# Kernel optimization log

Hardware: AMD Instinct MI355X
Metric: run time of the kernel (lower is better)

Reference implementation:

```python
import jax, jax.numpy as jnp
import numpy as np

CONTEXT_LENGTHS = [1, 3, 5, 7]
PADS = [(f - 1) // 2 for f in CONTEXT_LENGTHS]  # p(f) for odd f
B, H, L, DK = 2, 8, 1024, 64
C = H * DK  # conv channels = d_k * n_heads


def _conv1d(x, w, b, pad):
    # x: (b, C, L), w: (C, C, f), b: (C,) -- torch Conv1d semantics
    y = jax.lax.conv_general_dilated(
        x, w, window_strides=(1,), padding=[(pad, pad)],
        dimension_numbers=("NCH", "OIH", "NCH"))
    return y + b[None, :, None]


def _plane(a, w, b, pad, out_len):
    # Faithful to: conv(a.reshape(b, h*d_k, -1)).reshape(b, h, -1, d_k)[:, :, :out_len, :]
    bsz, h, l, d = a.shape
    y = _conv1d(a.reshape(bsz, h * d, l), w, b, pad)
    return y.reshape(bsz, h, -1, d)[:, :, :out_len, :]


def setup_inputs() -> dict:
    key = jax.random.key(0)
    ks = jax.random.split(key, 12)
    inp = {
        "Q": jax.random.normal(ks[0], (B, H, L, DK), jnp.float32),
        "K": jax.random.normal(ks[1], (B, H, L, DK), jnp.float32),
        "V": jax.random.normal(ks[2], (B, H, L, DK), jnp.float32),
        # causal mask: True = masked
        "attn_mask": jnp.broadcast_to(
            jnp.triu(jnp.ones((L, L), jnp.bool_), k=1), (B, H, L, L)),
    }
    for i, f in enumerate(CONTEXT_LENGTHS):
        scale = 1.0 / np.sqrt(C * f)
        inp[f"conv_w{i}"] = jax.random.normal(ks[3 + i], (C, C, f), jnp.float32) * scale
        inp[f"conv_b{i}"] = jax.random.normal(ks[7 + i], (C,), jnp.float32) * scale
    return inp


def reference(Q, K, V, attn_mask,
              conv_w0, conv_b0, conv_w1, conv_b1,
              conv_w2, conv_b2, conv_w3, conv_b3):
    ws = [conv_w0, conv_w1, conv_w2, conv_w3]
    bs = [conv_b0, conv_b1, conv_b2, conv_b3]
    b, h, l, d_k = Q.shape
    l_k = K.shape[2]
    p = len(CONTEXT_LENGTHS)
    Q_l = [_plane(Q, ws[i], bs[i], PADS[i], l) for i in range(p)]
    K_l = [_plane(K, ws[i], bs[i], PADS[i], l_k) for i in range(p)]
    # replicate torch.cat(dim=0).reshape(b, h, p, l, d) exactly (row-major)
    Q_p = jnp.concatenate(Q_l, axis=0).reshape(b, h, p, l, d_k)
    K_p = jnp.concatenate(K_l, axis=0).reshape(b, h, p, l_k, d_k)
    scores = jnp.einsum("bhpqd,bhpkd->bhpqk", Q_p, K_p) / np.sqrt(d_k).astype(np.float32)
    scores = jnp.where(attn_mask[:, :, None, :, :], jnp.float32(-1e9), scores)
    attn = jax.nn.softmax(scores, axis=-1)
    attn = jnp.max(attn, axis=2)  # max over planes -> (b,h,q,k)
    context = jnp.einsum("bhqk,bhkd->bhqd", attn, V)
    return (context, attn)
```

## Files before the change

kernel.cpp:

```cpp
#include <hip/hip_runtime.h>
#include <math.h>

#define C_CH 512
#define L_SEQ 1024
#define DK 64
#define NP 4

typedef __attribute__((ext_vector_type(8))) short short8;
typedef __attribute__((ext_vector_type(4))) float f32x4;

__device__ __forceinline__ unsigned short f2bf(float f) {
    union { float f; unsigned u; } v; v.f = f;
    unsigned u = v.u;
    u += 0x7FFFu + ((u >> 16) & 1u);
    return (unsigned short)(u >> 16);
}

__global__ __launch_bounds__(256)
void prep_w_kernel(const float* __restrict__ w0, const float* __restrict__ w1,
                   const float* __restrict__ w2, const float* __restrict__ w3,
                   unsigned short* __restrict__ Wb) {
    int tg = blockIdx.y;
    int plane, t;
    if (tg < 1)      { plane = 0; t = tg; }
    else if (tg < 4) { plane = 1; t = tg - 1; }
    else if (tg < 9) { plane = 2; t = tg - 4; }
    else             { plane = 3; t = tg - 9; }
    const float* W = (plane == 0) ? w0 : (plane == 1) ? w1 : (plane == 2) ? w2 : w3;
    const int f = (plane == 0) ? 1 : (plane == 1) ? 3 : (plane == 2) ? 5 : 7;

    int co = blockIdx.x * 32 + (threadIdx.x >> 3);
    int c8 = threadIdx.x & 7;
    for (int it = 0; it < 8; it++) {
        int ci = c8 * 8 + it * 64;
        unsigned short o[8];
#pragma unroll
        for (int j = 0; j < 8; j++)
            o[j] = f2bf(W[(size_t)(co * C_CH + ci + j) * f + t]);
        *(short8*)&Wb[((size_t)tg * C_CH + co) * C_CH + ci] = *(short8*)o;
    }
}

__global__ __launch_bounds__(256)
void prep_x_kernel(const float* __restrict__ Qin, const float* __restrict__ Kin,
                   unsigned short* __restrict__ Xt) {
    int tb = blockIdx.z;
    int tensor = tb >> 1, b = tb & 1;
    const float* X = (tensor ? Kin : Qin) + (size_t)b * C_CH * L_SEQ;
    unsigned short* O = Xt + (size_t)tb * 1032 * C_CH;

    int pos0 = blockIdx.x * 64;
    int ci0  = blockIdx.y * 64;
    int tid = threadIdx.x;

    __shared__ float tile[64][65];
    int tx = tid & 15, ty = tid >> 4;
#pragma unroll
    for (int rr = 0; rr < 4; rr++) {
        int ci_l = ty + rr * 16;
        float4 v = *(const float4*)&X[(size_t)(ci0 + ci_l) * L_SEQ + pos0 + tx * 4];
        tile[tx * 4 + 0][ci_l] = v.x;
        tile[tx * 4 + 1][ci_l] = v.y;
        tile[tx * 4 + 2][ci_l] = v.z;
        tile[tx * 4 + 3][ci_l] = v.w;
    }
    __syncthreads();
#pragma unroll
    for (int pp = 0; pp < 2; pp++) {
        int pos_l = (tid >> 3) + pp * 32;
        int cg = (tid & 7) * 8;
        unsigned short o[8];
#pragma unroll
        for (int j = 0; j < 8; j++) o[j] = f2bf(tile[pos_l][cg + j]);
        *(short8*)&O[(size_t)(pos0 + pos_l + 4) * C_CH + ci0 + cg] = *(short8*)o;
    }
    if (blockIdx.x == 0) {
        int r = tid >> 6, cc = tid & 63;
        O[(size_t)r * C_CH + ci0 + cc] = 0;
    }
    if (blockIdx.x == 15) {
        int r = tid >> 6, cc = tid & 63;
        O[(size_t)(1028 + r) * C_CH + ci0 + cc] = 0;
    }
}

__global__ __launch_bounds__(256)
void conv_mfma_kernel(const unsigned short* __restrict__ Xt,
                      const unsigned short* __restrict__ Wb,
                      const float* __restrict__ b0, const float* __restrict__ b1,
                      const float* __restrict__ b2, const float* __restrict__ b3,
                      unsigned short* __restrict__ Qp, unsigned short* __restrict__ Kp) {
    const int fs[4]   = {1, 3, 5, 7};
    const int toff[4] = {0, 1, 4, 9};
    int combo  = blockIdx.x;
    int b      = combo & 1;
    int plane  = (combo >> 1) & 3;
    int tensor = combo >> 3;
    const int f   = fs[plane];
    const int pad = (f - 1) >> 1;
    const float* bias = (plane == 0) ? b0 : (plane == 1) ? b1 : (plane == 2) ? b2 : b3;
    unsigned short* Out = tensor ? Kp : Qp;
    const unsigned short* Xbase = Xt + (size_t)(tensor * 2 + b) * 1032 * C_CH;

    int pos0 = blockIdx.y * 128;
    int co0  = blockIdx.z * 128;

    __shared__ __align__(16) unsigned short As[128 * 40];
    __shared__ __align__(16) unsigned short Bs[128 * 40];

    int tid  = threadIdx.x;
    int w    = tid >> 6;
    int lane = tid & 63;
    int l15  = lane & 15;
    int quad = lane >> 4;
    int wm = (w & 1) * 64;
    int wn = (w >> 1) * 64;

    int rowS = tid >> 2;
    int cS   = tid & 3;

    f32x4 acc[4][4];
#pragma unroll
    for (int mi = 0; mi < 4; mi++)
#pragma unroll
        for (int ni = 0; ni < 4; ni++) acc[mi][ni] = (f32x4){0.f, 0.f, 0.f, 0.f};

    for (int t = 0; t < f; t++) {
        const unsigned short* Wsl = Wb + ((size_t)(toff[plane] + t) * C_CH + co0) * C_CH;
        const unsigned short* Xsl = Xbase + (size_t)(pos0 + t - pad + 4) * C_CH;
        for (int cc = 0; cc < 16; cc++) {
            int kb = cc * 32;
            __syncthreads();
#pragma unroll
            for (int rep = 0; rep < 2; rep++) {
                int row = rowS + rep * 64;
                short8 va = *(const short8*)&Wsl[(size_t)row * C_CH + kb + cS * 8];
                *(short8*)&As[row * 40 + cS * 8] = va;
                short8 vb = *(const short8*)&Xsl[(size_t)row * C_CH + kb + cS * 8];
                *(short8*)&Bs[row * 40 + cS * 8] = vb;
            }
            __syncthreads();

            short8 af[4], bf[4];
#pragma unroll
            for (int mi = 0; mi < 4; mi++)
                af[mi] = *(const short8*)&As[(wm + mi * 16 + l15) * 40 + quad * 8];
#pragma unroll
            for (int ni = 0; ni < 4; ni++)
                bf[ni] = *(const short8*)&Bs[(wn + ni * 16 + l15) * 40 + quad * 8];
#pragma unroll
            for (int mi = 0; mi < 4; mi++)
#pragma unroll
                for (int ni = 0; ni < 4; ni++)
                    acc[mi][ni] = __builtin_amdgcn_mfma_f32_16x16x32_bf16(
                        af[mi], bf[ni], acc[mi][ni], 0, 0, 0);
        }
    }

#pragma unroll
    for (int mi = 0; mi < 4; mi++)
#pragma unroll
        for (int r = 0; r < 4; r++) {
            int co_l = wm + mi * 16 + quad * 4 + r;
            int co = co0 + co_l;
            int h = co >> 6, cl = co & 63;
            float bv = bias[co];
            size_t sbase = (size_t)((b * 8 + h) * NP + plane) * L_SEQ * DK;
#pragma unroll
            for (int ni = 0; ni < 4; ni++) {
                int pos = pos0 + wn + ni * 16 + l15;
                int l = cl * 16 + (pos >> 6);
                int d = pos & 63;
                Out[sbase + (size_t)l * DK + d] = f2bf(acc[mi][ni][r] + bv);
            }
        }
}

__global__ __launch_bounds__(256)
void attn_ctx_mfma(const unsigned short* __restrict__ Qb,
                   const unsigned short* __restrict__ Kb,
                   const float* __restrict__ V,
                   float* __restrict__ out_ctx, float* __restrict__ out_attn) {
    int qt = blockIdx.x, bh = blockIdx.y;
    int q0 = qt * 64;
    int b2 = bh >> 3, h2 = bh & 7;
    int plane  = b2 * 2 + (h2 >> 2);
    int b_orig = (h2 >> 1) & 1;
    int h_base = (h2 & 1) * 4;

    int tid  = threadIdx.x;
    int w    = tid >> 6;
    int lane = tid & 63;
    int l15  = lane & 15;
    int quad = lane >> 4;

    __shared__ __align__(16) unsigned short ast[64 * 80];
    __shared__ __align__(16) unsigned short vts[64 * 80];

    const unsigned short* kbase[NP];
    short8 qa[NP][2];
#pragma unroll
    for (int p = 0; p < NP; p++) {
        size_t slice = (size_t)((b_orig * 8 + h_base + p) * NP + plane);
        kbase[p] = Kb + slice * L_SEQ * DK;
        const unsigned short* qrow =
            Qb + (slice * L_SEQ + (size_t)(q0 + w * 16 + l15)) * DK + quad * 8;
        qa[p][0] = *(const short8*)(qrow);
        qa[p][1] = *(const short8*)(qrow + 32);
    }

    float m[NP][4], l[NP][4];
#pragma unroll
    for (int p = 0; p < NP; p++)
        for (int r = 0; r < 4; r++) { m[p][r] = -1e30f; l[p][r] = 0.f; }

    for (int kt = 0; kt <= qt; kt++) {
        int k0 = kt * 64;
        bool diag = (kt == qt);
#pragma unroll
        for (int p = 0; p < NP; p++) {
            f32x4 c[4];
#pragma unroll
            for (int s = 0; s < 4; s++) {
                const unsigned short* kr =
                    kbase[p] + (size_t)(k0 + s * 16 + l15) * DK + quad * 8;
                short8 kb0 = *(const short8*)(kr);
                short8 kb1 = *(const short8*)(kr + 32);
                f32x4 acc = {0.f, 0.f, 0.f, 0.f};
                acc = __builtin_amdgcn_mfma_f32_16x16x32_bf16(qa[p][0], kb0, acc, 0, 0, 0);
                acc = __builtin_amdgcn_mfma_f32_16x16x32_bf16(qa[p][1], kb1, acc, 0, 0, 0);
                c[s] = acc;
            }
#pragma unroll
            for (int r = 0; r < 4; r++) {
                int row_local = quad * 4 + r + w * 16;
                float sv[4];
                float tm = -1e30f;
#pragma unroll
                for (int s = 0; s < 4; s++) {
                    float x = c[s][r] * 0.125f;
                    if (diag && (s * 16 + l15 > row_local)) x = -1e30f;
                    sv[s] = x;
                    tm = fmaxf(tm, x);
                }
                float mo = m[p][r];
                float mn = fmaxf(mo, tm);
                float fac = __expf(mo - mn);
                float add = __expf(sv[0] - mn) + __expf(sv[1] - mn) +
                            __expf(sv[2] - mn) + __expf(sv[3] - mn);
                m[p][r] = mn;
                l[p][r] = l[p][r] * fac + add;
            }
        }
    }

    float mrow[NP][4], inv[NP][4];
#pragma unroll
    for (int p = 0; p < NP; p++)
#pragma unroll
        for (int r = 0; r < 4; r++) {
            float mm = m[p][r];
            mm = fmaxf(mm, __shfl_xor(mm, 1));
            mm = fmaxf(mm, __shfl_xor(mm, 2));
            mm = fmaxf(mm, __shfl_xor(mm, 4));
            mm = fmaxf(mm, __shfl_xor(mm, 8));
            float ll = l[p][r] * __expf(m[p][r] - mm);
            ll += __shfl_xor(ll, 1);
            ll += __shfl_xor(ll, 2);
            ll += __shfl_xor(ll, 4);
            ll += __shfl_xor(ll, 8);
            mrow[p][r] = mm;
            inv[p][r]  = 1.f / ll;
        }

    f32x4 ctxc[4];
#pragma unroll
    for (int ds = 0; ds < 4; ds++) ctxc[ds] = (f32x4){0.f, 0.f, 0.f, 0.f};

    for (int kt = 0; kt <= qt; kt++) {
        int k0 = kt * 64;
        bool diag = (kt == qt);
        float aval[4][4];
#pragma unroll
        for (int s = 0; s < 4; s++)
            for (int r = 0; r < 4; r++) aval[s][r] = 0.f;

#pragma unroll
        for (int p = 0; p < NP; p++) {
            f32x4 c[4];
#pragma unroll
            for (int s = 0; s < 4; s++) {
                const unsigned short* kr =
                    kbase[p] + (size_t)(k0 + s * 16 + l15) * DK + quad * 8;
                short8 kb0 = *(const short8*)(kr);
                short8 kb1 = *(const short8*)(kr + 32);
                f32x4 acc = {0.f, 0.f, 0.f, 0.f};
                acc = __builtin_amdgcn_mfma_f32_16x16x32_bf16(qa[p][0], kb0, acc, 0, 0, 0);
                acc = __builtin_amdgcn_mfma_f32_16x16x32_bf16(qa[p][1], kb1, acc, 0, 0, 0);
                c[s] = acc;
            }
#pragma unroll
            for (int r = 0; r < 4; r++) {
                int row_local = quad * 4 + r + w * 16;
#pragma unroll
                for (int s = 0; s < 4; s++) {
                    float x = c[s][r] * 0.125f;
                    if (diag && (s * 16 + l15 > row_local)) x = -1e30f;
                    float e = __expf(x - mrow[p][r]) * inv[p][r];
                    aval[s][r] = fmaxf(aval[s][r], e);
                }
            }
        }

#pragma unroll
        for (int s = 0; s < 4; s++)
#pragma unroll
            for (int r = 0; r < 4; r++) {
                int qloc = w * 16 + quad * 4 + r;
                int kg   = k0 + s * 16 + l15;
                out_attn[((size_t)bh * L_SEQ + q0 + qloc) * L_SEQ + kg] = aval[s][r];
                ast[qloc * 80 + s * 16 + l15] = f2bf(aval[s][r]);
            }

        {
            int kl = tid >> 2, db = (tid & 3) * 16;
            const float* vr = V + ((size_t)bh * L_SEQ + k0 + kl) * DK + db;
            float vv[16];
            *(float4*)&vv[0]  = *(const float4*)(vr);
            *(float4*)&vv[4]  = *(const float4*)(vr + 4);
            *(float4*)&vv[8]  = *(const float4*)(vr + 8);
            *(float4*)&vv[12] = *(const float4*)(vr + 12);
#pragma unroll
            for (int j = 0; j < 16; j++)
                vts[(db + j) * 80 + kl] = f2bf(vv[j]);
        }
        __syncthreads();

        short8 af0 = *(const short8*)&ast[(w * 16 + l15) * 80 + quad * 8];
        short8 af1 = *(const short8*)&ast[(w * 16 + l15) * 80 + 32 + quad * 8];
#pragma unroll
        for (int ds = 0; ds < 4; ds++) {
            short8 bf0 = *(const short8*)&vts[(ds * 16 + l15) * 80 + quad * 8];
            short8 bf1 = *(const short8*)&vts[(ds * 16 + l15) * 80 + 32 + quad * 8];
            ctxc[ds] = __builtin_amdgcn_mfma_f32_16x16x32_bf16(af0, bf0, ctxc[ds], 0, 0, 0);
            ctxc[ds] = __builtin_amdgcn_mfma_f32_16x16x32_bf16(af1, bf1, ctxc[ds], 0, 0, 0);
        }
        __syncthreads();
    }

    {
        int kz = (qt + 1) * 64;
        int ql = tid >> 2;
        float4 z = make_float4(0.f, 0.f, 0.f, 0.f);
        for (int k = kz + (tid & 3) * 4; k < L_SEQ; k += 16)
            *(float4*)&out_attn[((size_t)bh * L_SEQ + q0 + ql) * L_SEQ + k] = z;
    }

#pragma unroll
    for (int ds = 0; ds < 4; ds++)
#pragma unroll
        for (int r = 0; r < 4; r++) {
            int qg = q0 + w * 16 + quad * 4 + r;
            out_ctx[((size_t)bh * L_SEQ + qg) * DK + ds * 16 + l15] = ctxc[ds][r];
        }
}

extern "C" void kernel_launch(void* const* d_in, const int* in_sizes, int n_in,
                              void* d_out, int out_size, void* d_ws, size_t ws_size,
                              hipStream_t stream) {
    const float* Q  = (const float*)d_in[0];
    const float* K  = (const float*)d_in[1];
    const float* V  = (const float*)d_in[2];
    const float* w0 = (const float*)d_in[4];
    const float* b0 = (const float*)d_in[5];
    const float* w1 = (const float*)d_in[6];
    const float* b1 = (const float*)d_in[7];
    const float* w2 = (const float*)d_in[8];
    const float* b2 = (const float*)d_in[9];
    const float* w3 = (const float*)d_in[10];
    const float* b3 = (const float*)d_in[11];

    char* ws = (char*)d_ws;
    unsigned short* Wb = (unsigned short*)(ws);
    unsigned short* Xt = (unsigned short*)(ws + 8388608);
    unsigned short* Qp = (unsigned short*)(ws + 12615680);
    unsigned short* Kp = (unsigned short*)(ws + 21004288);

    float* out_ctx  = (float*)d_out;
    float* out_attn = out_ctx + 1048576;

    prep_w_kernel<<<dim3(16, 16), 256, 0, stream>>>(w0, w1, w2, w3, Wb);
    prep_x_kernel<<<dim3(16, 8, 4), 256, 0, stream>>>(Q, K, Xt);
    conv_mfma_kernel<<<dim3(16, 8, 4), 256, 0, stream>>>(Xt, Wb, b0, b1, b2, b3, Qp, Kp);
    attn_ctx_mfma<<<dim3(16, 16), 256, 0, stream>>>(Qp, Kp, V, out_ctx, out_attn);
}
```

Baseline: 425.2 us.

## Split causal attention into stats, combine and per-tile apply kernels

The single attention kernel, which ran one block per query tile serially over key tiles, becomes three kernels. A split-K stats pass computes partial softmax max and sum per key chunk, a combine kernel merges them and zeroes the context, and an apply kernel runs one block per (key tile, query tile) pair, writing attention and accumulating context with atomic adds. The aim is to fix the load imbalance and low occupancy of the causal loop (only 256 blocks with widely varying work). In exchange it adds two launches, atomic float adds whose summation order is nondeterministic, and workspace reuse over the Xt region.

After: 393.6 us. 1.08x faster.

```diff
diff --git a/kernel.cpp b/kernel.cpp
--- a/kernel.cpp
+++ b/kernel.cpp
@@ -177,25 +177,24 @@
 }
 
 __global__ __launch_bounds__(256)
-void attn_ctx_mfma(const unsigned short* __restrict__ Qb,
-                   const unsigned short* __restrict__ Kb,
-                   const float* __restrict__ V,
-                   float* __restrict__ out_ctx, float* __restrict__ out_attn) {
-    int qt = blockIdx.x, bh = blockIdx.y;
+void attn_stats_kernel(const unsigned short* __restrict__ Qb,
+                       const unsigned short* __restrict__ Kb,
+                       float2* __restrict__ pstats) {
+    int kc = blockIdx.x, qt = blockIdx.y, bh = blockIdx.z;
+    int tid = threadIdx.x;
+    size_t pbase = ((size_t)(bh * 16 + qt) * 4 + kc) * (NP * 64);
+
+    if (kc * 4 > qt) {
+        pstats[pbase + tid] = make_float2(-1e30f, 0.f);
+        return;
+    }
+
     int q0 = qt * 64;
     int b2 = bh >> 3, h2 = bh & 7;
     int plane  = b2 * 2 + (h2 >> 2);
     int b_orig = (h2 >> 1) & 1;
     int h_base = (h2 & 1) * 4;
-
-    int tid  = threadIdx.x;
-    int w    = tid >> 6;
-    int lane = tid & 63;
-    int l15  = lane & 15;
-    int quad = lane >> 4;
-
-    __shared__ __align__(16) unsigned short ast[64 * 80];
-    __shared__ __align__(16) unsigned short vts[64 * 80];
+    int w = tid >> 6, lane = tid & 63, l15 = lane & 15, quad = lane >> 4;
 
     const unsigned short* kbase[NP];
     short8 qa[NP][2];
@@ -214,7 +213,8 @@
     for (int p = 0; p < NP; p++)
         for (int r = 0; r < 4; r++) { m[p][r] = -1e30f; l[p][r] = 0.f; }
 
-    for (int kt = 0; kt <= qt; kt++) {
+    int kt1 = min(kc * 4 + 3, qt);
+    for (int kt = kc * 4; kt <= kt1; kt++) {
         int k0 = kt * 64;
         bool diag = (kt == qt);
 #pragma unroll
@@ -254,7 +254,6 @@
         }
     }
 
-    float mrow[NP][4], inv[NP][4];
 #pragma unroll
     for (int p = 0; p < NP; p++)
 #pragma unroll
@@ -269,91 +268,153 @@
             ll += __shfl_xor(ll, 2);
             ll += __shfl_xor(ll, 4);
             ll += __shfl_xor(ll, 8);
-            mrow[p][r] = mm;
-            inv[p][r]  = 1.f / ll;
-        }
+            if (l15 == 0)
+                pstats[pbase + p * 64 + (w * 16 + quad * 4 + r)] = make_float2(mm, ll);
+        }
+}
+
+__global__ __launch_bounds__(256)
+void attn_combine_kernel(const float2* __restrict__ pstats,
+                         float2* __restrict__ fstats,
+                         float* __restrict__ out_ctx) {
+    int qt = blockIdx.x, bh = blockIdx.y;
+    int tid = threadIdx.x;
+    size_t base = ((size_t)(bh * 16 + qt) * 4) * (NP * 64);
+
+    float2 s[4];
+    float m = -1e30f;
+#pragma unroll
+    for (int kc = 0; kc < 4; kc++) {
+        s[kc] = pstats[base + (size_t)kc * (NP * 64) + tid];
+        m = fmaxf(m, s[kc].x);
+    }
+    float l = 0.f;
+#pragma unroll
+    for (int kc = 0; kc < 4; kc++)
+        l += s[kc].y * __expf(s[kc].x - m);
+    fstats[(size_t)(bh * 16 + qt) * (NP * 64) + tid] = make_float2(m, 1.f / l);
+
+    int r = tid >> 2, c = (tid & 3) * 16;
+    float4 z = make_float4(0.f, 0.f, 0.f, 0.f);
+    size_t cbase = ((size_t)bh * L_SEQ + qt * 64 + r) * DK + c;
+#pragma unroll
+    for (int j = 0; j < 4; j++)
+        *(float4*)&out_ctx[cbase + j * 4] = z;
+}
+
+__global__ __launch_bounds__(256)
+void attn_apply_kernel(const unsigned short* __restrict__ Qb,
+                       const unsigned short* __restrict__ Kb,
+                       const float* __restrict__ V,
+                       const float2* __restrict__ fstats,
+                       float* __restrict__ out_ctx, float* __restrict__ out_attn) {
+    int kt = blockIdx.x, qt = blockIdx.y, bh = blockIdx.z;
+    int tid = threadIdx.x;
+    int q0 = qt * 64, k0 = kt * 64;
+
+    if (kt > qt) {
+        float4 z = make_float4(0.f, 0.f, 0.f, 0.f);
+        size_t base = ((size_t)bh * L_SEQ + q0 + (tid >> 2)) * L_SEQ + k0 + (tid & 3) * 16;
+#pragma unroll
+        for (int j = 0; j < 4; j++)
+            *(float4*)&out_attn[base + j * 4] = z;
+        return;
+    }
+
+    int b2 = bh >> 3, h2 = bh & 7;
+    int plane  = b2 * 2 + (h2 >> 2);
+    int b_orig = (h2 >> 1) & 1;
+    int h_base = (h2 & 1) * 4;
+    int w = tid >> 6, lane = tid & 63, l15 = lane & 15, quad = lane >> 4;
+    bool diag = (kt == qt);
+
+    __shared__ float2 sstats[NP * 64];
+    __shared__ __align__(16) unsigned short ast[64 * 80];
+    __shared__ __align__(16) unsigned short vts[64 * 80];
+
+    sstats[tid] = fstats[(size_t)(bh * 16 + qt) * (NP * 64) + tid];
+
+    const unsigned short* kbase[NP];
+    short8 qa[NP][2];
+#pragma unroll
+    for (int p = 0; p < NP; p++) {
+        size_t slice = (size_t)((b_orig * 8 + h_base + p) * NP + plane);
+        kbase[p] = Kb + slice * L_SEQ * DK;
+        const unsigned short* qrow =
+            Qb + (slice * L_SEQ + (size_t)(q0 + w * 16 + l15)) * DK + quad * 8;
+        qa[p][0] = *(const short8*)(qrow);
+        qa[p][1] = *(const short8*)(qrow + 32);
+    }
+
+    {
+        int kl = tid >> 2, db = (tid & 3) * 16;
+        const float* vr = V + ((size_t)bh * L_SEQ + k0 + kl) * DK + db;
+        float vv[16];
+        *(float4*)&vv[0]  = *(const float4*)(vr);
+        *(float4*)&vv[4]  = *(const float4*)(vr + 4);
+        *(float4*)&vv[8]  = *(const float4*)(vr + 8);
+        *(float4*)&vv[12] = *(const float4*)(vr + 12);
+#pragma unroll
+        for (int j = 0; j < 16; j++)
+            vts[(db + j) * 80 + kl] = f2bf(vv[j]);
+    }
+    __syncthreads();
+
+    float aval[4][4];
+#pragma unroll
+    for (int s = 0; s < 4; s++)
+        for (int r = 0; r < 4; r++) aval[s][r] = 0.f;
+
+#pragma unroll
+    for (int p = 0; p < NP; p++) {
+        f32x4 c[4];
+#pragma unroll
+        for (int s = 0; s < 4; s++) {
+            const unsigned short* kr =
+                kbase[p] + (size_t)(k0 + s * 16 + l15) * DK + quad * 8;
+            short8 kb0 = *(const short8*)(kr);
+            short8 kb1 = *(const short8*)(kr + 32);
+            f32x4 acc = {0.f, 0.f, 0.f, 0.f};
+            acc = __builtin_amdgcn_mfma_f32_16x16x32_bf16(qa[p][0], kb0, acc, 0, 0, 0);
+            acc = __builtin_amdgcn_mfma_f32_16x16x32_bf16(qa[p][1], kb1, acc, 0, 0, 0);
+            c[s] = acc;
+        }
+#pragma unroll
+        for (int r = 0; r < 4; r++) {
+            int row_local = quad * 4 + r + w * 16;
+            float2 st = sstats[p * 64 + row_local];
+#pragma unroll
+            for (int s = 0; s < 4; s++) {
+                float x = c[s][r] * 0.125f;
+                if (diag && (s * 16 + l15 > row_local)) x = -1e30f;
+                float e = __expf(x - st.x) * st.y;
+                aval[s][r] = fmaxf(aval[s][r], e);
+            }
+        }
+    }
+
+#pragma unroll
+    for (int s = 0; s < 4; s++)
+#pragma unroll
+        for (int r = 0; r < 4; r++) {
+            int qloc = w * 16 + quad * 4 + r;
+            int kg   = k0 + s * 16 + l15;
+            out_attn[((size_t)bh * L_SEQ + q0 + qloc) * L_SEQ + kg] = aval[s][r];
+            ast[qloc * 80 + s * 16 + l15] = f2bf(aval[s][r]);
+        }
+    __syncthreads();
 
     f32x4 ctxc[4];
 #pragma unroll
     for (int ds = 0; ds < 4; ds++) ctxc[ds] = (f32x4){0.f, 0.f, 0.f, 0.f};
-
-    for (int kt = 0; kt <= qt; kt++) {
-        int k0 = kt * 64;
-        bool diag = (kt == qt);
-        float aval[4][4];
-#pragma unroll
-        for (int s = 0; s < 4; s++)
-            for (int r = 0; r < 4; r++) aval[s][r] = 0.f;
-
-#pragma unroll
-        for (int p = 0; p < NP; p++) {
-            f32x4 c[4];
-#pragma unroll
-            for (int s = 0; s < 4; s++) {
-                const unsigned short* kr =
-                    kbase[p] + (size_t)(k0 + s * 16 + l15) * DK + quad * 8;
-                short8 kb0 = *(const short8*)(kr);
-                short8 kb1 = *(const short8*)(kr + 32);
-                f32x4 acc = {0.f, 0.f, 0.f, 0.f};
-                acc = __builtin_amdgcn_mfma_f32_16x16x32_bf16(qa[p][0], kb0, acc, 0, 0, 0);
-                acc = __builtin_amdgcn_mfma_f32_16x16x32_bf16(qa[p][1], kb1, acc, 0, 0, 0);
-                c[s] = acc;
-            }
-#pragma unroll
-            for (int r = 0; r < 4; r++) {
-                int row_local = quad * 4 + r + w * 16;
-#pragma unroll
-                for (int s = 0; s < 4; s++) {
-                    float x = c[s][r] * 0.125f;
-                    if (diag && (s * 16 + l15 > row_local)) x = -1e30f;
-                    float e = __expf(x - mrow[p][r]) * inv[p][r];
-                    aval[s][r] = fmaxf(aval[s][r], e);
-                }
-            }
-        }
-
-#pragma unroll
-        for (int s = 0; s < 4; s++)
-#pragma unroll
-            for (int r = 0; r < 4; r++) {
-                int qloc = w * 16 + quad * 4 + r;
-                int kg   = k0 + s * 16 + l15;
-                out_attn[((size_t)bh * L_SEQ + q0 + qloc) * L_SEQ + kg] = aval[s][r];
-                ast[qloc * 80 + s * 16 + l15] = f2bf(aval[s][r]);
-            }
-
-        {
-            int kl = tid >> 2, db = (tid & 3) * 16;
-            const float* vr = V + ((size_t)bh * L_SEQ + k0 + kl) * DK + db;
-            float vv[16];
-            *(float4*)&vv[0]  = *(const float4*)(vr);
-            *(float4*)&vv[4]  = *(const float4*)(vr + 4);
-            *(float4*)&vv[8]  = *(const float4*)(vr + 8);
-            *(float4*)&vv[12] = *(const float4*)(vr + 12);
-#pragma unroll
-            for (int j = 0; j < 16; j++)
-                vts[(db + j) * 80 + kl] = f2bf(vv[j]);
-        }
-        __syncthreads();
-
-        short8 af0 = *(const short8*)&ast[(w * 16 + l15) * 80 + quad * 8];
-        short8 af1 = *(const short8*)&ast[(w * 16 + l15) * 80 + 32 + quad * 8];
-#pragma unroll
-        for (int ds = 0; ds < 4; ds++) {
-            short8 bf0 = *(const short8*)&vts[(ds * 16 + l15) * 80 + quad * 8];
-            short8 bf1 = *(const short8*)&vts[(ds * 16 + l15) * 80 + 32 + quad * 8];
-            ctxc[ds] = __builtin_amdgcn_mfma_f32_16x16x32_bf16(af0, bf0, ctxc[ds], 0, 0, 0);
-            ctxc[ds] = __builtin_amdgcn_mfma_f32_16x16x32_bf16(af1, bf1, ctxc[ds], 0, 0, 0);
-        }
-        __syncthreads();
-    }
-
-    {
-        int kz = (qt + 1) * 64;
-        int ql = tid >> 2;
-        float4 z = make_float4(0.f, 0.f, 0.f, 0.f);
-        for (int k = kz + (tid & 3) * 4; k < L_SEQ; k += 16)
-            *(float4*)&out_attn[((size_t)bh * L_SEQ + q0 + ql) * L_SEQ + k] = z;
+    short8 af0 = *(const short8*)&ast[(w * 16 + l15) * 80 + quad * 8];
+    short8 af1 = *(const short8*)&ast[(w * 16 + l15) * 80 + 32 + quad * 8];
+#pragma unroll
+    for (int ds = 0; ds < 4; ds++) {
+        short8 bf0 = *(const short8*)&vts[(ds * 16 + l15) * 80 + quad * 8];
+        short8 bf1 = *(const short8*)&vts[(ds * 16 + l15) * 80 + 32 + quad * 8];
+        ctxc[ds] = __builtin_amdgcn_mfma_f32_16x16x32_bf16(af0, bf0, ctxc[ds], 0, 0, 0);
+        ctxc[ds] = __builtin_amdgcn_mfma_f32_16x16x32_bf16(af1, bf1, ctxc[ds], 0, 0, 0);
     }
 
 #pragma unroll
@@ -361,7 +422,8 @@
 #pragma unroll
         for (int r = 0; r < 4; r++) {
             int qg = q0 + w * 16 + quad * 4 + r;
-            out_ctx[((size_t)bh * L_SEQ + qg) * DK + ds * 16 + l15] = ctxc[ds][r];
+            unsafeAtomicAdd(&out_ctx[((size_t)bh * L_SEQ + qg) * DK + ds * 16 + l15],
+                            ctxc[ds][r]);
         }
 }
 
@@ -385,6 +447,8 @@
     unsigned short* Xt = (unsigned short*)(ws + 8388608);
     unsigned short* Qp = (unsigned short*)(ws + 12615680);
     unsigned short* Kp = (unsigned short*)(ws + 21004288);
+    float2* pstats = (float2*)(ws + 8388608);
+    float2* fstats = (float2*)(ws + 8388608 + 2097152);
 
     float* out_ctx  = (float*)d_out;
     float* out_attn = out_ctx + 1048576;
@@ -392,5 +456,8 @@
     prep_w_kernel<<<dim3(16, 16), 256, 0, stream>>>(w0, w1, w2, w3, Wb);
     prep_x_kernel<<<dim3(16, 8, 4), 256, 0, stream>>>(Q, K, Xt);
     conv_mfma_kernel<<<dim3(16, 8, 4), 256, 0, stream>>>(Xt, Wb, b0, b1, b2, b3, Qp, Kp);
-    attn_ctx_mfma<<<dim3(16, 16), 256, 0, stream>>>(Qp, Kp, V, out_ctx, out_attn);
-}
+    attn_stats_kernel<<<dim3(4, 16, 16), 256, 0, stream>>>(Qp, Kp, pstats);
+    attn_combine_kernel<<<dim3(16, 16), 256, 0, stream>>>(pstats, fstats, out_ctx);
+    attn_apply_kernel<<<dim3(16, 16, 16), 256, 0, stream>>>(Qp, Kp, V, fstats,
+                                                            out_ctx, out_attn);
+}
```
